# Kernel tuning notes

Hardware: AMD Instinct MI355X
Metric: run time of the kernel (lower is better)

Reference implementation:

```python
import jax, jax.numpy as jnp
import numpy as np

N_GROUP = 8
N_ITER = 3


def setup_inputs() -> dict:
    key = jax.random.key(0)
    x = jax.random.normal(key, (16, 64, 64, 512), dtype=jnp.float32)
    return {"x": x}


def reference(x):
    # x: [B, H, W, G*C] NHWC feature map
    B, H, W, Cg = x.shape
    G = N_GROUP
    C = Cg // G
    xr = x.reshape(B, H, W, G, C)  # [B,H,W,G,C]
    # routing logits per (batch, group); broadcastable against xr
    beta = jnp.zeros((B, 1, 1, G, 1), dtype=x.dtype)
    v = jnp.zeros((B, H, W, 1, C), dtype=x.dtype)
    for i in range(N_ITER):
        alpha = jax.nn.sigmoid(beta)                      # [B,1,1,G,1]
        v = jnp.sum(alpha * xr, axis=-2, keepdims=True)   # [B,H,W,1,C]
        if i < N_ITER - 1:
            # agreement: reduce over spatial dims and channels -> per (batch, group)
            beta = beta + jnp.sum(v * xr, axis=(1, 2, 4), keepdims=True)
    return v[..., 0, :]  # [B,H,W,C]
```

## Files before the change

kernel.cpp:

```cpp
#include <hip/hip_runtime.h>
#include <math.h>

#define BATCH   16
#define HW      4096
#define CG      512
#define NPAIR   36
#define F4_PER_POS   128
#define F4_PER_GROUP 16
#define SLOTS_PER_B  65536
#define XB_F4        524288

__global__ __launch_bounds__(256) void gram_kernel(const float* __restrict__ xf,
                                                   float* __restrict__ S) {
    const float4* x = (const float4*)xf;
    const int b = blockIdx.y;
    const int stride = gridDim.x * 256;
    int t = blockIdx.x * 256 + threadIdx.x;

    float acc[NPAIR];
#pragma unroll
    for (int p = 0; p < NPAIR; ++p) acc[p] = 0.f;

    const float4* xb = x + (long)b * XB_F4;
    for (int slot = t; slot < SLOTS_PER_B; slot += stride) {
        const int pos = slot >> 4;
        const int c4  = slot & 15;
        const float4* ptr = xb + pos * F4_PER_POS + c4;
        float4 xg[8];
#pragma unroll
        for (int g = 0; g < 8; ++g) xg[g] = ptr[g * F4_PER_GROUP];
        int p = 0;
#pragma unroll
        for (int g = 0; g < 8; ++g) {
#pragma unroll
            for (int gp = g; gp < 8; ++gp, ++p) {
                acc[p] += xg[g].x * xg[gp].x + xg[g].y * xg[gp].y +
                          xg[g].z * xg[gp].z + xg[g].w * xg[gp].w;
            }
        }
    }

#pragma unroll
    for (int p = 0; p < NPAIR; ++p) {
        float v = acc[p];
#pragma unroll
        for (int off = 32; off; off >>= 1) v += __shfl_xor(v, off, 64);
        acc[p] = v;
    }

    __shared__ float red[4][NPAIR];
    const int lane = threadIdx.x & 63;
    const int wave = threadIdx.x >> 6;
    if (lane == 0) {
#pragma unroll
        for (int p = 0; p < NPAIR; ++p) red[wave][p] = acc[p];
    }
    __syncthreads();
    if (threadIdx.x < NPAIR) {
        float v = red[0][threadIdx.x] + red[1][threadIdx.x] +
                  red[2][threadIdx.x] + red[3][threadIdx.x];
        atomicAdd(&S[b * NPAIR + threadIdx.x], v);
    }
}

__global__ __launch_bounds__(256) void out_kernel(const float* __restrict__ xf,
                                                  const float* __restrict__ S,
                                                  float* __restrict__ outf) {
    const float4* x = (const float4*)xf;
    float4* out = (float4*)outf;
    const int b   = blockIdx.x >> 8;
    const int blk = blockIdx.x & 255;

    __shared__ float alpha1s[8];
    __shared__ float alpha2s[8];

    const int g = threadIdx.x;
    float row[8];
    float beta1 = 0.f;
    if (g < 8) {
#pragma unroll
        for (int gp = 0; gp < 8; ++gp) {
            const int a  = g < gp ? g : gp;
            const int bb = g < gp ? gp : g;
            const int idx = a * 8 - (a * (a - 1)) / 2 + (bb - a);
            row[gp] = S[b * NPAIR + idx];
            beta1 += row[gp];
        }
        beta1 *= 0.5f;
        alpha1s[g] = 1.f / (1.f + expf(-beta1));
    }
    __syncthreads();
    if (g < 8) {
        float beta2 = beta1;
#pragma unroll
        for (int gp = 0; gp < 8; ++gp) beta2 += alpha1s[gp] * row[gp];
        alpha2s[g] = 1.f / (1.f + expf(-beta2));
    }
    __syncthreads();

    float a[8];
#pragma unroll
    for (int gg = 0; gg < 8; ++gg) a[gg] = alpha2s[gg];

    const int t   = blk * 256 + threadIdx.x;
    const int pos = t >> 4;
    const int c4  = t & 15;
    const float4* ptr = x + (long)b * XB_F4 + pos * F4_PER_POS + c4;

    float4 accv = make_float4(0.f, 0.f, 0.f, 0.f);
#pragma unroll
    for (int gg = 0; gg < 8; ++gg) {
        const float4 v = ptr[gg * F4_PER_GROUP];
        accv.x += a[gg] * v.x;
        accv.y += a[gg] * v.y;
        accv.z += a[gg] * v.z;
        accv.w += a[gg] * v.w;
    }
    out[(long)b * SLOTS_PER_B + t] = accv;
}

extern "C" void kernel_launch(void* const* d_in, const int* in_sizes, int n_in,
                              void* d_out, int out_size, void* d_ws, size_t ws_size,
                              hipStream_t stream) {
    const float* x = (const float*)d_in[0];
    float* out = (float*)d_out;
    float* S = (float*)d_ws;

    hipMemsetAsync(S, 0, BATCH * NPAIR * sizeof(float), stream);

    dim3 g1(64, BATCH);
    gram_kernel<<<g1, 256, 0, stream>>>(x, S);
    out_kernel<<<BATCH * 256, 256, 0, stream>>>(x, S, out);
}
```

Measured before the change: 217.1 us.

## Replace atomic Gram accumulation with per-block partials and drop the memset

The Gram kernel now writes per-block partial sums to the workspace instead of doing atomicAdd, so the hipMemsetAsync launch goes away. The output kernel reduces the 64 partials per batch in shared memory, and each of its blocks now handles four times as much work (1024 blocks instead of 4096). This removes one launch and the atomic contention. In exchange, every output block redundantly re-reduces 64x36 partials, and the output grid has fewer blocks to hide latency with.

```diff
diff --git a/kernel.cpp b/kernel.cpp
--- a/kernel.cpp
+++ b/kernel.cpp
@@ -1,30 +1,31 @@
 #include <hip/hip_runtime.h>
 #include <math.h>
 
-#define BATCH   16
-#define HW      4096
-#define CG      512
-#define NPAIR   36
+#define BATCH        16
+#define NPAIR        36
 #define F4_PER_POS   128
 #define F4_PER_GROUP 16
 #define SLOTS_PER_B  65536
 #define XB_F4        524288
+#define BLOCKS_PER_B 64
+#define NBLOCKS      (BATCH * BLOCKS_PER_B)
 
 __global__ __launch_bounds__(256) void gram_kernel(const float* __restrict__ xf,
-                                                   float* __restrict__ S) {
+                                                   float* __restrict__ partials) {
     const float4* x = (const float4*)xf;
-    const int b = blockIdx.y;
-    const int stride = gridDim.x * 256;
-    int t = blockIdx.x * 256 + threadIdx.x;
+    const int b   = blockIdx.x >> 6;
+    const int blk = blockIdx.x & 63;
+    const float4* xb = x + (long)b * XB_F4;
 
     float acc[NPAIR];
 #pragma unroll
     for (int p = 0; p < NPAIR; ++p) acc[p] = 0.f;
 
-    const float4* xb = x + (long)b * XB_F4;
-    for (int slot = t; slot < SLOTS_PER_B; slot += stride) {
-        const int pos = slot >> 4;
-        const int c4  = slot & 15;
+#pragma unroll
+    for (int it = 0; it < 4; ++it) {
+        const int t   = blk * 1024 + it * 256 + threadIdx.x;
+        const int pos = t >> 4;
+        const int c4  = t & 15;
         const float4* ptr = xb + pos * F4_PER_POS + c4;
         float4 xg[8];
 #pragma unroll
@@ -57,22 +58,33 @@
     }
     __syncthreads();
     if (threadIdx.x < NPAIR) {
-        float v = red[0][threadIdx.x] + red[1][threadIdx.x] +
-                  red[2][threadIdx.x] + red[3][threadIdx.x];
-        atomicAdd(&S[b * NPAIR + threadIdx.x], v);
+        partials[blockIdx.x * NPAIR + threadIdx.x] =
+            red[0][threadIdx.x] + red[1][threadIdx.x] +
+            red[2][threadIdx.x] + red[3][threadIdx.x];
     }
 }
 
 __global__ __launch_bounds__(256) void out_kernel(const float* __restrict__ xf,
-                                                  const float* __restrict__ S,
+                                                  const float* __restrict__ partials,
                                                   float* __restrict__ outf) {
     const float4* x = (const float4*)xf;
     float4* out = (float4*)outf;
-    const int b   = blockIdx.x >> 8;
-    const int blk = blockIdx.x & 255;
+    const int b   = blockIdx.x >> 6;
+    const int blk = blockIdx.x & 63;
+    const float4* xb = x + (long)b * XB_F4;
 
+    __shared__ float Sred[NPAIR];
     __shared__ float alpha1s[8];
     __shared__ float alpha2s[8];
+
+    if (threadIdx.x < NPAIR) {
+        float s = 0.f;
+        const float* pb = partials + (long)b * BLOCKS_PER_B * NPAIR + threadIdx.x;
+#pragma unroll 8
+        for (int j = 0; j < BLOCKS_PER_B; ++j) s += pb[j * NPAIR];
+        Sred[threadIdx.x] = s;
+    }
+    __syncthreads();
 
     const int g = threadIdx.x;
     float row[8];
@@ -83,7 +95,7 @@
             const int a  = g < gp ? g : gp;
             const int bb = g < gp ? gp : g;
             const int idx = a * 8 - (a * (a - 1)) / 2 + (bb - a);
-            row[gp] = S[b * NPAIR + idx];
+            row[gp] = Sred[idx];
             beta1 += row[gp];
         }
         beta1 *= 0.5f;
@@ -102,21 +114,23 @@
 #pragma unroll
     for (int gg = 0; gg < 8; ++gg) a[gg] = alpha2s[gg];
 
-    const int t   = blk * 256 + threadIdx.x;
-    const int pos = t >> 4;
-    const int c4  = t & 15;
-    const float4* ptr = x + (long)b * XB_F4 + pos * F4_PER_POS + c4;
-
-    float4 accv = make_float4(0.f, 0.f, 0.f, 0.f);
 #pragma unroll
-    for (int gg = 0; gg < 8; ++gg) {
-        const float4 v = ptr[gg * F4_PER_GROUP];
-        accv.x += a[gg] * v.x;
-        accv.y += a[gg] * v.y;
-        accv.z += a[gg] * v.z;
-        accv.w += a[gg] * v.w;
+    for (int it = 0; it < 4; ++it) {
+        const int t   = blk * 1024 + it * 256 + threadIdx.x;
+        const int pos = t >> 4;
+        const int c4  = t & 15;
+        const float4* ptr = xb + pos * F4_PER_POS + c4;
+        float4 accv = make_float4(0.f, 0.f, 0.f, 0.f);
+#pragma unroll
+        for (int gg = 0; gg < 8; ++gg) {
+            const float4 v = ptr[gg * F4_PER_GROUP];
+            accv.x += a[gg] * v.x;
+            accv.y += a[gg] * v.y;
+            accv.z += a[gg] * v.z;
+            accv.w += a[gg] * v.w;
+        }
+        out[(long)b * SLOTS_PER_B + t] = accv;
     }
-    out[(long)b * SLOTS_PER_B + t] = accv;
 }
 
 extern "C" void kernel_launch(void* const* d_in, const int* in_sizes, int n_in,
@@ -124,11 +138,8 @@
                               hipStream_t stream) {
     const float* x = (const float*)d_in[0];
     float* out = (float*)d_out;
-    float* S = (float*)d_ws;
+    float* partials = (float*)d_ws;
 
-    hipMemsetAsync(S, 0, BATCH * NPAIR * sizeof(float), stream);
-
-    dim3 g1(64, BATCH);
-    gram_kernel<<<g1, 256, 0, stream>>>(x, S);
-    out_kernel<<<BATCH * 256, 256, 0, stream>>>(x, S, out);
+    gram_kernel<<<NBLOCKS, 256, 0, stream>>>(x, partials);
+    out_kernel<<<NBLOCKS, 256, 0, stream>>>(x, partials, out);
 }
```

Measured after the change: 220.1 us. No clear change (+1.4%).
